# Kernel optimization log

Measured on AMD Instinct MI355X. Metric: run time of the kernel, lower is better.

Reference implementation:

```python
import jax, jax.numpy as jnp
import numpy as np

N_EMBD = 1024
N_HEAD = 16
HEAD_DIM = N_EMBD // N_HEAD


def setup_inputs() -> dict:
    key = jax.random.key(0)
    ks = jax.random.split(key, 8)
    B, T, T_ctx, C = 2, 2048, 2048, N_EMBD
    s = 1.0 / np.sqrt(C)
    return {
        "x": jax.random.normal(ks[0], (B, T, C), dtype=jnp.float32),
        "context": jax.random.normal(ks[1], (B, T_ctx, C), dtype=jnp.float32),
        # Linear weights stored as [in, out] (torch stores [out, in]; math identical via x @ W)
        "Wq": jax.random.normal(ks[2], (C, C), dtype=jnp.float32) * s,
        "bq": jnp.zeros((C,), dtype=jnp.float32),
        "Wkv": jax.random.normal(ks[3], (C, 2 * C), dtype=jnp.float32) * s,
        "bkv": jnp.zeros((2 * C,), dtype=jnp.float32),
        "Wp": jax.random.normal(ks[4], (C, C), dtype=jnp.float32) * s,
        "bp": jnp.zeros((C,), dtype=jnp.float32),
    }


def reference(x, context, Wq, bq, Wkv, bkv, Wp, bp):
    B, T, C = x.shape
    T_ctx = context.shape[1]
    H, D = N_HEAD, C // N_HEAD

    q = (x @ Wq + bq).reshape(B, T, H, D).transpose(0, 2, 1, 3)          # [B,H,T,D]
    kv = context @ Wkv + bkv                                             # [B,T_ctx,2C]
    k, v = jnp.split(kv, 2, axis=-1)
    k = k.reshape(B, T_ctx, H, D).transpose(0, 2, 1, 3)                  # [B,H,T_ctx,D]
    v = v.reshape(B, T_ctx, H, D).transpose(0, 2, 1, 3)                  # [B,H,T_ctx,D]

    att = jnp.einsum("bhtd,bhsd->bhts", q, k) * (1.0 / jnp.sqrt(jnp.asarray(D, q.dtype)))
    # tril(ones(T, T_ctx)): position t attends to context positions s <= t
    causal = jnp.arange(T)[:, None] >= jnp.arange(T_ctx)[None, :]        # [T,T_ctx]
    att = jnp.where(causal[None, None], att, jnp.asarray(-jnp.inf, att.dtype))
    att = jax.nn.softmax(att, axis=-1)

    y = jnp.einsum("bhts,bhsd->bhtd", att, v)                            # [B,H,T,D]
    y = y.transpose(0, 2, 1, 3).reshape(B, T, C)
    return y @ Wp + bp
```

## Files before the change

kernel.cpp:

```cpp
#include <hip/hip_runtime.h>
#include <hip/hip_bf16.h>

typedef __bf16 bf16;
typedef __bf16 bf16x8 __attribute__((ext_vector_type(8)));
typedef __bf16 bf16x4 __attribute__((ext_vector_type(4)));
typedef float f32x4 __attribute__((ext_vector_type(4)));
typedef float f32x16 __attribute__((ext_vector_type(16)));

#define GLOAD_LDS16(g, l) \
  __builtin_amdgcn_global_load_lds((const __attribute__((address_space(1))) void*)(g), \
                                   (__attribute__((address_space(3))) void*)(l), 16, 0, 0)

static __device__ __forceinline__ unsigned cvtpk_bf16(float lo, float hi) {
  unsigned r;
  asm("v_cvt_pk_bf16_f32 %0, %1, %2" : "=v"(r) : "v"(lo), "v"(hi));
  return r;
}
static __device__ __forceinline__ void pl32swap(unsigned& a, unsigned& b) {
  asm volatile("v_permlane32_swap_b32 %0, %1" : "+v"(a), "+v"(b));
}

__global__ __launch_bounds__(256) void prep_kernel(
    const float* __restrict__ x, const float* __restrict__ ctx,
    const float* __restrict__ Wq, const float* __restrict__ Wkv, const float* __restrict__ Wp,
    bf16* __restrict__ x_bf, bf16* __restrict__ c_bf,
    bf16* __restrict__ Wq_t, bf16* __restrict__ Wkv_t, bf16* __restrict__ Wp_t) {
  const int bid = blockIdx.x;
  if (bid < 8192) {
    const int i = (bid & 4095) * 256 + threadIdx.x;
    const float4 v = (bid < 4096) ? ((const float4*)x)[i] : ((const float4*)ctx)[i];
    bf16x4 o;
    o.x = (bf16)v.x; o.y = (bf16)v.y; o.z = (bf16)v.z; o.w = (bf16)v.w;
    if (bid < 4096) ((bf16x4*)x_bf)[i] = o; else ((bf16x4*)c_bf)[i] = o;
    return;
  }
  __shared__ float tile[32][33];
  int tb = bid - 8192;
  const float* W; bf16* Wt; int N;
  if (tb < 1024) { W = Wq; Wt = Wq_t; N = 1024; }
  else if (tb < 3072) { W = Wkv; Wt = Wkv_t; N = 2048; tb -= 1024; }
  else { W = Wp; Wt = Wp_t; N = 1024; tb -= 3072; }
  const int nt = N >> 5;
  const int n0 = (tb % nt) * 32, k0 = (tb / nt) * 32;
  const int tx = threadIdx.x & 31, ty = threadIdx.x >> 5;
#pragma unroll
  for (int i = 0; i < 32; i += 8)
    tile[ty + i][tx] = W[(size_t)(k0 + ty + i) * N + n0 + tx];
  __syncthreads();
#pragma unroll
  for (int i = 0; i < 32; i += 8)
    Wt[(size_t)(n0 + ty + i) * 1024 + k0 + tx] = (bf16)tile[tx][ty + i];
}

__global__ __launch_bounds__(256) void proj_gemm_kernel(
    const bf16* __restrict__ x_bf, const bf16* __restrict__ c_bf,
    const bf16* __restrict__ Wq_t, const bf16* __restrict__ Wkv_t,
    const float* __restrict__ bq, const float* __restrict__ bkv,
    bf16* __restrict__ Qh, bf16* __restrict__ Kh, bf16* __restrict__ Vt) {
  __shared__ __align__(16) bf16 As[128 * 32];
  __shared__ __align__(16) bf16 Bs[64 * 32];
  __shared__ __align__(16) bf16 Vb[64 * 128];

  const int tid = threadIdx.x;
  const int lane = tid & 63;
  const int w = tid >> 6;
  const int wr = w >> 1, wc = w & 1;
  const int g4 = lane >> 4, r16 = lane & 15;

  int bid = blockIdx.x;
  bid = (bid & 7) * 192 + (bid >> 3);
  const bool isq = bid < 512;
  const int lid = isq ? bid : bid - 512;
  const int gX = isq ? 16 : 32;
  const int bx = lid % gX, by = lid / gX;
  const int m0 = by * 128, n0 = bx * 64;
  const bf16* A = isq ? x_bf : c_bf;
  const bf16* Bt = isq ? Wq_t : Wkv_t;
  const float* bias = isq ? bq : bkv;

  const bf16* Ag0 = A + (size_t)(m0 + (tid >> 2)) * 1024 + (tid & 3) * 8;
  const bf16* Ag1 = A + (size_t)(m0 + 64 + (tid >> 2)) * 1024 + (tid & 3) * 8;
  const bf16* Bg0 = Bt + (size_t)(n0 + (tid >> 2)) * 1024 + (tid & 3) * 8;
  const int wu = __builtin_amdgcn_readfirstlane(w);
  bf16* As0 = As + wu * 512;
  bf16* As1 = As + 2048 + wu * 512;
  bf16* Bs0 = Bs + wu * 512;

  f32x4 acc[4][2] = {};

  for (int k0 = 0; k0 < 1024; k0 += 32) {
    __syncthreads();
    GLOAD_LDS16(Ag0 + k0, As0);
    GLOAD_LDS16(Ag1 + k0, As1);
    GLOAD_LDS16(Bg0 + k0, Bs0);
    __syncthreads();
    bf16x8 af[4], bfr[2];
#pragma unroll
    for (int i = 0; i < 4; i++)
      af[i] = *(const bf16x8*)(As + (wr * 64 + i * 16 + r16) * 32 + g4 * 8);
#pragma unroll
    for (int i = 0; i < 2; i++)
      bfr[i] = *(const bf16x8*)(Bs + (wc * 32 + i * 16 + r16) * 32 + g4 * 8);
#pragma unroll
    for (int mi = 0; mi < 4; mi++)
#pragma unroll
      for (int ni = 0; ni < 2; ni++)
        acc[mi][ni] = __builtin_amdgcn_mfma_f32_16x16x32_bf16(af[mi], bfr[ni], acc[mi][ni], 0, 0, 0);
  }

  if (!isq && n0 >= 1024) {
    __syncthreads();
#pragma unroll
    for (int mi = 0; mi < 4; mi++)
#pragma unroll
      for (int ni = 0; ni < 2; ni++) {
        const float bv = bias[n0 + wc * 32 + ni * 16 + r16];
#pragma unroll
        for (int r = 0; r < 4; r++)
          Vb[(wc * 32 + ni * 16 + r16) * 128 + wr * 64 + mi * 16 + 4 * g4 + r] =
              (bf16)(acc[mi][ni][r] + bv);
      }
    __syncthreads();
    const int bb = m0 >> 11, t0l = m0 & 2047;
    const int c2base = n0 - 1024;
#pragma unroll
    for (int p = 0; p < 4; ++p) {
      const int slot = tid + p * 256;
      const int d = slot >> 4, j = slot & 15;
      const int c2 = c2base + d;
      const int h = c2 >> 6, dd = c2 & 63;
      *(bf16x8*)(Vt + ((size_t)((bb * 16 + h) * 64 + dd)) * 2048 + t0l + j * 8) =
          *(const bf16x8*)(Vb + d * 128 + j * 8);
    }
    return;
  }

#pragma unroll
  for (int mi = 0; mi < 4; mi++) {
#pragma unroll
    for (int ni = 0; ni < 2; ni++) {
      const int col = n0 + wc * 32 + ni * 16 + r16;
      const float bv = bias[col];
      const int rowb = m0 + wr * 64 + mi * 16 + 4 * g4;
#pragma unroll
      for (int r = 0; r < 4; r++) {
        const int row = rowb + r;
        const float v = acc[mi][ni][r] + bv;
        const int bb = row >> 11, t = row & 2047;
        const int h = col >> 6, d = col & 63;
        if (isq)
          Qh[((size_t)(bb * 16 + h) * 2048 + t) * 64 + d] = (bf16)(v * 0.18033688f);
        else
          Kh[((size_t)(bb * 16 + h) * 2048 + t) * 64 + d] = (bf16)v;
      }
    }
  }
}

__global__ __launch_bounds__(256) void gemm_out_kernel(
    const bf16* __restrict__ A, const bf16* __restrict__ Bt,
    const float* __restrict__ bias, float* __restrict__ out) {
  __shared__ __align__(16) bf16 As[128 * 32];
  __shared__ __align__(16) bf16 Bs[64 * 32];

  const int tid = threadIdx.x;
  const int lane = tid & 63;
  const int w = tid >> 6;
  const int wr = w >> 1, wc = w & 1;
  const int g4 = lane >> 4, r16 = lane & 15;

  int bid = blockIdx.x;
  bid = (bid & 7) * 64 + (bid >> 3);
  const int bx = bid & 15, by = bid >> 4;
  const int m0 = by * 128, n0 = bx * 64;

  const bf16* Ag0 = A + (size_t)(m0 + (tid >> 2)) * 1024 + (tid & 3) * 8;
  const bf16* Ag1 = A + (size_t)(m0 + 64 + (tid >> 2)) * 1024 + (tid & 3) * 8;
  const bf16* Bg0 = Bt + (size_t)(n0 + (tid >> 2)) * 1024 + (tid & 3) * 8;
  const int wu = __builtin_amdgcn_readfirstlane(w);
  bf16* As0 = As + wu * 512;
  bf16* As1 = As + 2048 + wu * 512;
  bf16* Bs0 = Bs + wu * 512;

  f32x4 acc[4][2] = {};

  for (int k0 = 0; k0 < 1024; k0 += 32) {
    __syncthreads();
    GLOAD_LDS16(Ag0 + k0, As0);
    GLOAD_LDS16(Ag1 + k0, As1);
    GLOAD_LDS16(Bg0 + k0, Bs0);
    __syncthreads();
    bf16x8 af[4], bfr[2];
#pragma unroll
    for (int i = 0; i < 4; i++)
      af[i] = *(const bf16x8*)(As + (wr * 64 + i * 16 + r16) * 32 + g4 * 8);
#pragma unroll
    for (int i = 0; i < 2; i++)
      bfr[i] = *(const bf16x8*)(Bs + (wc * 32 + i * 16 + r16) * 32 + g4 * 8);
#pragma unroll
    for (int mi = 0; mi < 4; mi++)
#pragma unroll
      for (int ni = 0; ni < 2; ni++)
        acc[mi][ni] = __builtin_amdgcn_mfma_f32_16x16x32_bf16(af[mi], bfr[ni], acc[mi][ni], 0, 0, 0);
  }

#pragma unroll
  for (int mi = 0; mi < 4; mi++)
#pragma unroll
    for (int ni = 0; ni < 2; ni++) {
      const int col = n0 + wc * 32 + ni * 16 + r16;
      const float bv = bias[col];
      const int rowb = m0 + wr * 64 + mi * 16 + 4 * g4;
#pragma unroll
      for (int r = 0; r < 4; r++)
        out[(size_t)(rowb + r) * 1024 + col] = acc[mi][ni][r] + bv;
    }
}

#define AE2(c, tb, te, sl) ((c) | ((tb) << 3) | ((te) << 9) | ((sl) << 15))
__constant__ int ATAB[12] = {
  AE2(7, 0, 16, 6), AE2(7, 16, 32, 7), AE2(3, 0, 16, 0),
  AE2(6, 0, 14, 4), AE2(6, 14, 28, 5), AE2(5, 0, 12, 2),
  AE2(5, 12, 24, 3), AE2(2, 0, 12, 0), AE2(4, 0, 10, 0),
  AE2(4, 10, 20, 1), AE2(1, 0, 8, 0),  AE2(0, 0, 4, 0),
};

__global__ __launch_bounds__(512) void attn_kernel(
    const bf16* __restrict__ Q, const bf16* __restrict__ Kh,
    const bf16* __restrict__ Vt, bf16* __restrict__ Y,
    bf16* __restrict__ Po, float* __restrict__ Lsum) {
  __shared__ __align__(16) bf16 Kls[2][4096];
  __shared__ __align__(16) bf16 Vls[2][4096];

  const int tid = threadIdx.x;
  const int lane = tid & 63;
  const int w = tid >> 6;
  const int l31 = lane & 31;
  const int g = lane >> 5;
  const int u = blockIdx.x >> 5;
  const int bh = blockIdx.x & 31;
  const int e = ATAB[u];
  const int c = e & 7, tb = (e >> 3) & 63, te = (e >> 9) & 63, slot = (e >> 15) & 7;
  const int slotg = bh * 8 + slot;
  const bool single = (tb == 0) && (te == 4 * c + 4);
  const int b = bh >> 4, h = bh & 15;
  const int qb = c * 256;
  const int wq = qb + w * 32;
  const int wu = __builtin_amdgcn_readfirstlane(w);

  bf16x8 qf[4];
  {
    const bf16* qp = Q + ((size_t)bh * 2048 + wq + l31) * 64 + g * 8;
#pragma unroll
    for (int cc = 0; cc < 4; ++cc) qf[cc] = *(const bf16x8*)(qp + cc * 16);
  }

  f32x16 O0 = {}, O1 = {};
  float l = 0.f;

  auto stage = [&](int bi, int s0) {
    const int s = tid >> 3, j = tid & 7;
    const int js = (j ^ (s & 7)) * 8;
    GLOAD_LDS16(Kh + ((size_t)bh * 2048 + s0 + s) * 64 + js, &Kls[bi][wu * 512]);
    GLOAD_LDS16(Vt + ((size_t)bh * 64 + s) * 2048 + s0 + js, &Vls[bi][wu * 512]);
  };

  stage(tb & 1, tb * 64);

  for (int t = tb; t < te; ++t) {
    const int s0 = t * 64;
    asm volatile("s_waitcnt vmcnt(0)" ::: "memory");
    __builtin_amdgcn_s_barrier();
    asm volatile("" ::: "memory");
    if (t + 1 < te) stage((t + 1) & 1, s0 + 64);

    if (s0 < wq + 32) {
      const bf16* Kb = Kls[t & 1];
      const bf16* Vb = Vls[t & 1];

      f32x16 SA = {}, SB = {};
      __builtin_amdgcn_s_setprio(1);
#pragma unroll
      for (int cc = 0; cc < 4; ++cc) {
        const int sl = ((cc * 2 + g) ^ (l31 & 7)) * 8;
        bf16x8 kf0 = *(const bf16x8*)(Kb + l31 * 64 + sl);
        SA = __builtin_amdgcn_mfma_f32_32x32x16_bf16(kf0, qf[cc], SA, 0, 0, 0);
        bf16x8 kf1 = *(const bf16x8*)(Kb + (32 + l31) * 64 + sl);
        SB = __builtin_amdgcn_mfma_f32_32x32x16_bf16(kf1, qf[cc], SB, 0, 0, 0);
      }
      __builtin_amdgcn_s_setprio(0);

      const int qg = wq + l31;
      if (s0 + 63 > wq) {
#pragma unroll
        for (int r = 0; r < 16; ++r) {
          const int sl = (r & 3) + 8 * (r >> 2) + 4 * g;
          SA[r] = (s0 + sl <= qg) ? SA[r] : -3.0e38f;
          SB[r] = (s0 + 32 + sl <= qg) ? SB[r] : -3.0e38f;
        }
      }

      float ps = 0.f;
#pragma unroll
      for (int r = 0; r < 16; ++r) { SA[r] = __builtin_amdgcn_exp2f(SA[r]); ps += SA[r]; }
#pragma unroll
      for (int r = 0; r < 16; ++r) { SB[r] = __builtin_amdgcn_exp2f(SB[r]); ps += SB[r]; }
      l += ps;

      union PW { unsigned u[4]; bf16x8 v; };
      PW pa0, pa1, pa2, pa3;
      {
        unsigned A0 = cvtpk_bf16(SA[0], SA[1]), B0 = cvtpk_bf16(SA[2], SA[3]);
        unsigned C0 = cvtpk_bf16(SA[4], SA[5]), D0 = cvtpk_bf16(SA[6], SA[7]);
        pl32swap(A0, C0); pl32swap(B0, D0);
        pa0.u[0] = A0; pa0.u[1] = B0; pa0.u[2] = C0; pa0.u[3] = D0;

        unsigned A1 = cvtpk_bf16(SA[8], SA[9]), B1 = cvtpk_bf16(SA[10], SA[11]);
        unsigned C1 = cvtpk_bf16(SA[12], SA[13]), D1 = cvtpk_bf16(SA[14], SA[15]);
        pl32swap(A1, C1); pl32swap(B1, D1);
        pa1.u[0] = A1; pa1.u[1] = B1; pa1.u[2] = C1; pa1.u[3] = D1;

        unsigned A2 = cvtpk_bf16(SB[0], SB[1]), B2 = cvtpk_bf16(SB[2], SB[3]);
        unsigned C2 = cvtpk_bf16(SB[4], SB[5]), D2 = cvtpk_bf16(SB[6], SB[7]);
        pl32swap(A2, C2); pl32swap(B2, D2);
        pa2.u[0] = A2; pa2.u[1] = B2; pa2.u[2] = C2; pa2.u[3] = D2;

        unsigned A3 = cvtpk_bf16(SB[8], SB[9]), B3 = cvtpk_bf16(SB[10], SB[11]);
        unsigned C3 = cvtpk_bf16(SB[12], SB[13]), D3 = cvtpk_bf16(SB[14], SB[15]);
        pl32swap(A3, C3); pl32swap(B3, D3);
        pa3.u[0] = A3; pa3.u[1] = B3; pa3.u[2] = C3; pa3.u[3] = D3;
      }

      __builtin_amdgcn_s_setprio(1);
#pragma unroll
      for (int cc = 0; cc < 4; ++cc) {
        const bf16x8 pav = (cc == 0) ? pa0.v : (cc == 1) ? pa1.v : (cc == 2) ? pa2.v : pa3.v;
        const int sl = ((cc * 2 + g) ^ (l31 & 7)) * 8;
        bf16x8 vf0 = *(const bf16x8*)(Vb + l31 * 64 + sl);
        O0 = __builtin_amdgcn_mfma_f32_32x32x16_bf16(pav, vf0, O0, 0, 0, 0);
        bf16x8 vf1 = *(const bf16x8*)(Vb + (32 + l31) * 64 + sl);
        O1 = __builtin_amdgcn_mfma_f32_32x32x16_bf16(pav, vf1, O1, 0, 0, 0);
      }
      __builtin_amdgcn_s_setprio(0);
    }
  }

  l += __shfl_xor(l, 32, 64);
  if (!single && g == 0)
    Lsum[(size_t)slotg * 256 + w * 32 + l31] = l;
#pragma unroll
  for (int r = 0; r < 16; ++r) {
    const int qr = (r & 3) + 8 * (r >> 2) + (g << 2);
    const float lr = __shfl(l, qr, 64);
    const float inv = (lr > 0.f) ? 1.f / lr : 0.f;
    if (single) {
      const int tq = wq + qr;
      bf16* yp = Y + ((size_t)(b * 2048 + tq)) * 1024 + h * 64 + l31;
      yp[0]  = (bf16)(O0[r] * inv);
      yp[32] = (bf16)(O1[r] * inv);
    } else {
      bf16* pp = Po + (size_t)slotg * 16384 + (w * 32 + qr) * 64 + l31;
      pp[0]  = (bf16)(O0[r] * inv);
      pp[32] = (bf16)(O1[r] * inv);
    }
  }
}

__global__ __launch_bounds__(256) void attn_combine(
    const bf16* __restrict__ Po, const float* __restrict__ Lsum, bf16* __restrict__ Y) {
  const int bh = blockIdx.x >> 2, ci = blockIdx.x & 3;
  const int c = ci + 4;
  const int base = bh * 8 + ci * 2;
  const int b = bh >> 4, h = bh & 15;
  const int tid = threadIdx.x;
#pragma unroll
  for (int k = 0; k < 8; ++k) {
    const int tt = tid + k * 256;
    const int row = tt >> 3, cg = tt & 7;
    const float w0 = Lsum[(size_t)base * 256 + row];
    const float w1 = Lsum[(size_t)(base + 1) * 256 + row];
    const bf16x8 v0 = *(const bf16x8*)(Po + (size_t)base * 16384 + row * 64 + cg * 8);
    const bf16x8 v1 = *(const bf16x8*)(Po + (size_t)(base + 1) * 16384 + row * 64 + cg * 8);
    const float inv = 1.f / (w0 + w1);
    bf16x8 o;
#pragma unroll
    for (int j = 0; j < 8; ++j) o[j] = (bf16)((w0 * (float)v0[j] + w1 * (float)v1[j]) * inv);
    const int t = c * 256 + row;
    *(bf16x8*)(Y + ((size_t)(b * 2048 + t)) * 1024 + h * 64 + cg * 8) = o;
  }
}

extern "C" void kernel_launch(void* const* d_in, const int* in_sizes, int n_in,
                              void* d_out, int out_size, void* d_ws, size_t ws_size,
                              hipStream_t stream) {
  (void)in_sizes; (void)n_in; (void)out_size; (void)ws_size;
  const float* x   = (const float*)d_in[0];
  const float* ctx = (const float*)d_in[1];
  const float* Wq  = (const float*)d_in[2];
  const float* bq  = (const float*)d_in[3];
  const float* Wkv = (const float*)d_in[4];
  const float* bkv = (const float*)d_in[5];
  const float* Wp  = (const float*)d_in[6];
  const float* bp  = (const float*)d_in[7];
  float* out = (float*)d_out;

  char* ws = (char*)d_ws;
  const size_t MB = 1024 * 1024;
  bf16*  Po    = (bf16*)(ws + 0 * MB);
  float* Lsum  = (float*)(ws + 9 * MB);
  bf16* x_bf   = (bf16*)(ws + 0 * MB);
  bf16* c_bf   = (bf16*)(ws + 10 * MB);
  bf16* Wq_t   = (bf16*)(ws + 18 * MB);
  bf16* Wkv_t  = (bf16*)(ws + 20 * MB);
  bf16* Wp_t   = (bf16*)(ws + 24 * MB);
  bf16* Qh     = (bf16*)(ws + 26 * MB);
  bf16* Kh     = (bf16*)(ws + 34 * MB);
  bf16* Vt     = (bf16*)(ws + 42 * MB);
  bf16* y_bf   = (bf16*)(ws + 50 * MB);

  prep_kernel<<<12288, 256, 0, stream>>>(x, ctx, Wq, Wkv, Wp, x_bf, c_bf, Wq_t, Wkv_t, Wp_t);
  proj_gemm_kernel<<<1536, 256, 0, stream>>>(x_bf, c_bf, Wq_t, Wkv_t, bq, bkv, Qh, Kh, Vt);
  attn_kernel<<<384, 512, 0, stream>>>(Qh, Kh, Vt, y_bf, Po, Lsum);
  attn_combine<<<128, 256, 0, stream>>>(Po, Lsum, y_bf);
  gemm_out_kernel<<<512, 256, 0, stream>>>(y_bf, Wp_t, bp, out);
}
```

Measured before the change: 117.9 us.

## Rewrite QKV projection GEMM with 256x256 tiles, swizzled LDS and pipelined prefetch

The Q/KV projection GEMM moves from 128x64 tiles with 256 threads to 256x256 tiles with 512 threads (8 waves, each computing 128x64). The K loop uses 64-wide slices, XOR-swizzled LDS layout to avoid bank conflicts, and double buffering in which the next K-tile's quarter-loads are interleaved between MFMA quads. The goal is higher arithmetic intensity, fewer global reloads of A and B, and overlap of loads with compute. The cost is only 192 blocks on a 256-CU part, so some CUs sit idle, plus higher register and LDS pressure.

```diff
diff --git a/kernel.cpp b/kernel.cpp
--- a/kernel.cpp
+++ b/kernel.cpp
@@ -52,109 +52,182 @@
     Wt[(size_t)(n0 + ty + i) * 1024 + k0 + tx] = (bf16)tile[tx][ty + i];
 }
 
-__global__ __launch_bounds__(256) void proj_gemm_kernel(
+__global__ __launch_bounds__(512, 2) void proj_gemm8_kernel(
     const bf16* __restrict__ x_bf, const bf16* __restrict__ c_bf,
     const bf16* __restrict__ Wq_t, const bf16* __restrict__ Wkv_t,
     const float* __restrict__ bq, const float* __restrict__ bkv,
     bf16* __restrict__ Qh, bf16* __restrict__ Kh, bf16* __restrict__ Vt) {
-  __shared__ __align__(16) bf16 As[128 * 32];
-  __shared__ __align__(16) bf16 Bs[64 * 32];
-  __shared__ __align__(16) bf16 Vb[64 * 128];
+  __shared__ __align__(16) bf16 SMEM[67584];
+  bf16* AS = SMEM;
+  bf16* BS = SMEM + 32768;
 
   const int tid = threadIdx.x;
   const int lane = tid & 63;
   const int w = tid >> 6;
-  const int wr = w >> 1, wc = w & 1;
+  const int wm = w >> 2, wn = w & 3;
   const int g4 = lane >> 4, r16 = lane & 15;
+  const int wu = __builtin_amdgcn_readfirstlane(w);
 
   int bid = blockIdx.x;
-  bid = (bid & 7) * 192 + (bid >> 3);
-  const bool isq = bid < 512;
-  const int lid = isq ? bid : bid - 512;
-  const int gX = isq ? 16 : 32;
-  const int bx = lid % gX, by = lid / gX;
-  const int m0 = by * 128, n0 = bx * 64;
-  const bf16* A = isq ? x_bf : c_bf;
+  bid = (bid & 7) * 24 + (bid >> 3);
+  const bool isq = bid < 64;
+  const int lid = isq ? bid : bid - 64;
+  const int bx = isq ? (lid & 3) : (lid & 7);
+  const int by = isq ? (lid >> 2) : (lid >> 3);
+  const int m0 = by * 256, n0 = bx * 256;
+  const bf16* Am = isq ? x_bf : c_bf;
   const bf16* Bt = isq ? Wq_t : Wkv_t;
   const float* bias = isq ? bq : bkv;
 
-  const bf16* Ag0 = A + (size_t)(m0 + (tid >> 2)) * 1024 + (tid & 3) * 8;
-  const bf16* Ag1 = A + (size_t)(m0 + 64 + (tid >> 2)) * 1024 + (tid & 3) * 8;
-  const bf16* Bg0 = Bt + (size_t)(n0 + (tid >> 2)) * 1024 + (tid & 3) * 8;
-  const int wu = __builtin_amdgcn_readfirstlane(w);
-  bf16* As0 = As + wu * 512;
-  bf16* As1 = As + 2048 + wu * 512;
-  bf16* Bs0 = Bs + wu * 512;
-
-  f32x4 acc[4][2] = {};
-
-  for (int k0 = 0; k0 < 1024; k0 += 32) {
+  f32x4 acc[8][4] = {};
+  bf16x8 af[4][2];
+  bf16x8 bfr[2][2][2];
+
+#define STAGE_HT(which, kt)                                                          \
+  {                                                                                  \
+    const int kb_ = (kt) & 1;                                                        \
+    const int h_ = (which) & 1;                                                      \
+    const bf16* src_ = ((which) < 2) ? (Am + (size_t)(m0 + h_ * 128) * 1024)         \
+                                     : (Bt + (size_t)(n0 + h_ * 128) * 1024);        \
+    bf16* dst_ = (((which) < 2) ? AS : BS) + kb_ * 16384 + h_ * 8192;                \
+    const int k0_ = (kt) * 64;                                                       \
+    _Pragma("unroll")                                                                \
+    for (int run_ = 0; run_ < 2; ++run_) {                                           \
+      const int s_ = run_ * 512 + tid;                                               \
+      const int row_ = s_ >> 3, j_ = s_ & 7;                                         \
+      const int jj_ = j_ ^ (row_ & 7);                                               \
+      GLOAD_LDS16(src_ + (size_t)row_ * 1024 + k0_ + jj_ * 8,                        \
+                  dst_ + (run_ * 512 + wu * 64) * 8);                                \
+    }                                                                                \
+  }
+
+#define LDA(MH, KB)                                                                  \
+  {                                                                                  \
+    const bf16* Ah_ = AS + (KB) * 16384 + wm * 8192;                                 \
+    _Pragma("unroll")                                                                \
+    for (int mi_ = 0; mi_ < 4; ++mi_) {                                              \
+      const int lr_ = (MH) * 64 + mi_ * 16 + r16;                                    \
+      _Pragma("unroll")                                                              \
+      for (int kk_ = 0; kk_ < 2; ++kk_) {                                            \
+        const int jl_ = (kk_ * 4 + g4) ^ (lr_ & 7);                                  \
+        af[mi_][kk_] = *(const bf16x8*)(Ah_ + lr_ * 64 + jl_ * 8);                   \
+      }                                                                              \
+    }                                                                                \
+  }
+
+#define LDB(NH, KB)                                                                  \
+  {                                                                                  \
+    const bf16* Bh_ = BS + (KB) * 16384 + (wn >> 1) * 8192;                          \
+    _Pragma("unroll")                                                                \
+    for (int ni_ = 0; ni_ < 2; ++ni_) {                                              \
+      const int lr_ = (wn & 1) * 64 + (NH) * 32 + ni_ * 16 + r16;                    \
+      _Pragma("unroll")                                                              \
+      for (int kk_ = 0; kk_ < 2; ++kk_) {                                            \
+        const int jl_ = (kk_ * 4 + g4) ^ (lr_ & 7);                                  \
+        bfr[NH][ni_][kk_] = *(const bf16x8*)(Bh_ + lr_ * 64 + jl_ * 8);              \
+      }                                                                              \
+    }                                                                                \
+  }
+
+#define QUAD(MH, NH)                                                                 \
+  __builtin_amdgcn_s_setprio(1);                                                     \
+  _Pragma("unroll")                                                                  \
+  for (int mi_ = 0; mi_ < 4; ++mi_)                                                  \
+    _Pragma("unroll")                                                                \
+    for (int ni_ = 0; ni_ < 2; ++ni_) {                                              \
+      acc[(MH)*4 + mi_][(NH)*2 + ni_] = __builtin_amdgcn_mfma_f32_16x16x32_bf16(     \
+          af[mi_][0], bfr[NH][ni_][0], acc[(MH)*4 + mi_][(NH)*2 + ni_], 0, 0, 0);    \
+      acc[(MH)*4 + mi_][(NH)*2 + ni_] = __builtin_amdgcn_mfma_f32_16x16x32_bf16(     \
+          af[mi_][1], bfr[NH][ni_][1], acc[(MH)*4 + mi_][(NH)*2 + ni_], 0, 0, 0);    \
+    }                                                                                \
+  __builtin_amdgcn_s_setprio(0);
+
+#define PIN_AFTER_BARRIER()              \
+  __builtin_amdgcn_sched_barrier(0);     \
+  asm volatile("" ::: "memory");
+
+  STAGE_HT(0, 0); STAGE_HT(1, 0); STAGE_HT(2, 0); STAGE_HT(3, 0);
+
+  for (int j = 0; j < 16; ++j) {
+    const int kb = j & 1;
+    const bool pf = (j + 1 < 16);
+    if (pf) STAGE_HT(0, j + 1);
+    if (pf) { asm volatile("s_waitcnt vmcnt(2)" ::: "memory"); }
+    else    { asm volatile("s_waitcnt vmcnt(0)" ::: "memory"); }
+    __builtin_amdgcn_s_barrier();
+    PIN_AFTER_BARRIER();
+    LDA(0, kb); LDB(0, kb);
+    QUAD(0, 0);
+    if (pf) STAGE_HT(1, j + 1);
+    __builtin_amdgcn_s_barrier();
+    PIN_AFTER_BARRIER();
+    LDB(1, kb);
+    QUAD(0, 1);
+    if (pf) STAGE_HT(2, j + 1);
+    __builtin_amdgcn_s_barrier();
+    PIN_AFTER_BARRIER();
+    LDA(1, kb);
+    QUAD(1, 1);
+    if (pf) STAGE_HT(3, j + 1);
+    __builtin_amdgcn_s_barrier();
+    PIN_AFTER_BARRIER();
+    QUAD(1, 0);
+  }
+
+  if (isq || n0 < 1024) {
+#pragma unroll
+    for (int mf = 0; mf < 8; ++mf) {
+#pragma unroll
+      for (int nf = 0; nf < 4; ++nf) {
+        const int gc = n0 + wn * 64 + nf * 16 + r16;
+        const float bv = bias[gc];
+        const int h = gc >> 6, d = gc & 63;
+#pragma unroll
+        for (int r = 0; r < 4; ++r) {
+          const int gr = m0 + wm * 128 + mf * 16 + 4 * g4 + r;
+          const int bb = gr >> 11, t = gr & 2047;
+          const float v = acc[mf][nf][r] + bv;
+          if (isq)
+            Qh[((size_t)(bb * 16 + h) * 2048 + t) * 64 + d] = (bf16)(v * 0.18033688f);
+          else
+            Kh[((size_t)(bb * 16 + h) * 2048 + t) * 64 + d] = (bf16)v;
+        }
+      }
+    }
+  } else {
+    bf16* VL = SMEM;
     __syncthreads();
-    GLOAD_LDS16(Ag0 + k0, As0);
-    GLOAD_LDS16(Ag1 + k0, As1);
-    GLOAD_LDS16(Bg0 + k0, Bs0);
+#pragma unroll
+    for (int mf = 0; mf < 8; ++mf) {
+#pragma unroll
+      for (int nf = 0; nf < 4; ++nf) {
+        const int cl = wn * 64 + nf * 16 + r16;
+        const float bv = bias[n0 + cl];
+#pragma unroll
+        for (int r = 0; r < 4; ++r) {
+          const int rl = wm * 128 + mf * 16 + 4 * g4 + r;
+          VL[cl * 264 + rl] = (bf16)(acc[mf][nf][r] + bv);
+        }
+      }
+    }
     __syncthreads();
-    bf16x8 af[4], bfr[2];
-#pragma unroll
-    for (int i = 0; i < 4; i++)
-      af[i] = *(const bf16x8*)(As + (wr * 64 + i * 16 + r16) * 32 + g4 * 8);
-#pragma unroll
-    for (int i = 0; i < 2; i++)
-      bfr[i] = *(const bf16x8*)(Bs + (wc * 32 + i * 16 + r16) * 32 + g4 * 8);
-#pragma unroll
-    for (int mi = 0; mi < 4; mi++)
-#pragma unroll
-      for (int ni = 0; ni < 2; ni++)
-        acc[mi][ni] = __builtin_amdgcn_mfma_f32_16x16x32_bf16(af[mi], bfr[ni], acc[mi][ni], 0, 0, 0);
-  }
-
-  if (!isq && n0 >= 1024) {
-    __syncthreads();
-#pragma unroll
-    for (int mi = 0; mi < 4; mi++)
-#pragma unroll
-      for (int ni = 0; ni < 2; ni++) {
-        const float bv = bias[n0 + wc * 32 + ni * 16 + r16];
-#pragma unroll
-        for (int r = 0; r < 4; r++)
-          Vb[(wc * 32 + ni * 16 + r16) * 128 + wr * 64 + mi * 16 + 4 * g4 + r] =
-              (bf16)(acc[mi][ni][r] + bv);
-      }
-    __syncthreads();
+    const int col = tid >> 1;
+    const int rbase = (tid & 1) * 128;
+    const int c2 = n0 - 1024 + col;
+    const int h = c2 >> 6, d = c2 & 63;
     const int bb = m0 >> 11, t0l = m0 & 2047;
-    const int c2base = n0 - 1024;
-#pragma unroll
-    for (int p = 0; p < 4; ++p) {
-      const int slot = tid + p * 256;
-      const int d = slot >> 4, j = slot & 15;
-      const int c2 = c2base + d;
-      const int h = c2 >> 6, dd = c2 & 63;
-      *(bf16x8*)(Vt + ((size_t)((bb * 16 + h) * 64 + dd)) * 2048 + t0l + j * 8) =
-          *(const bf16x8*)(Vb + d * 128 + j * 8);
-    }
-    return;
-  }
-
-#pragma unroll
-  for (int mi = 0; mi < 4; mi++) {
-#pragma unroll
-    for (int ni = 0; ni < 2; ni++) {
-      const int col = n0 + wc * 32 + ni * 16 + r16;
-      const float bv = bias[col];
-      const int rowb = m0 + wr * 64 + mi * 16 + 4 * g4;
-#pragma unroll
-      for (int r = 0; r < 4; r++) {
-        const int row = rowb + r;
-        const float v = acc[mi][ni][r] + bv;
-        const int bb = row >> 11, t = row & 2047;
-        const int h = col >> 6, d = col & 63;
-        if (isq)
-          Qh[((size_t)(bb * 16 + h) * 2048 + t) * 64 + d] = (bf16)(v * 0.18033688f);
-        else
-          Kh[((size_t)(bb * 16 + h) * 2048 + t) * 64 + d] = (bf16)v;
-      }
-    }
-  }
+    bf16* vdst = Vt + ((size_t)((bb * 16 + h) * 64 + d)) * 2048 + t0l;
+#pragma unroll
+    for (int p = 0; p < 16; ++p) {
+      const int row = rbase + p * 8;
+      *(bf16x8*)(vdst + row) = *(const bf16x8*)(VL + col * 264 + row);
+    }
+  }
+#undef STAGE_HT
+#undef LDA
+#undef LDB
+#undef QUAD
+#undef PIN_AFTER_BARRIER
 }
 
 __global__ __launch_bounds__(256) void gemm_out_kernel(
@@ -419,7 +492,7 @@
   bf16* y_bf   = (bf16*)(ws + 50 * MB);
 
   prep_kernel<<<12288, 256, 0, stream>>>(x, ctx, Wq, Wkv, Wp, x_bf, c_bf, Wq_t, Wkv_t, Wp_t);
-  proj_gemm_kernel<<<1536, 256, 0, stream>>>(x_bf, c_bf, Wq_t, Wkv_t, bq, bkv, Qh, Kh, Vt);
+  proj_gemm8_kernel<<<192, 512, 0, stream>>>(x_bf, c_bf, Wq_t, Wkv_t, bq, bkv, Qh, Kh, Vt);
   attn_kernel<<<384, 512, 0, stream>>>(Qh, Kh, Vt, y_bf, Po, Lsum);
   attn_combine<<<128, 256, 0, stream>>>(Po, Lsum, y_bf);
   gemm_out_kernel<<<512, 256, 0, stream>>>(y_bf, Wp_t, bp, out);
```

After: 105.3 us. -10.7%, faster.
